# Kernel optimization log

Hardware: AMD Instinct MI355X
Metric: run time of the kernel (lower is better)

## Reference

```python
import jax, jax.numpy as jnp
import numpy as np

N, R, E = 20000, 4, 40000
C_IN, C_EDGE, HID, OUT = 256, 128, 512, 256
H = 8
D = HID // H
SCALE = 1.0 / float(np.sqrt(D))


def _hgt_layer(x, src, dst, Wkqv, bkqv, Wk, Wv, prel, Wout, bout, skip):
    # x: [n, c_in]; src/dst: [R, E] int; Wk/Wv: [R, H, D, D]; prel: [R, H]
    n = x.shape[0]
    kqv = x @ Wkqv + bkqv                      # [n, 3*HID], split order k|q|v (torch.tensor_split)
    k, q, v = jnp.split(kqv, 3, axis=1)
    k = k.reshape(n, H, D)
    q = q.reshape(n, H, D)
    v = v.reshape(n, H, D)
    # per-(relation, head) DxD transforms (HeteroLinear k_rel / v_rel, no bias)
    k_rel = jnp.einsum('nhd,rhde->rnhe', k, Wk)   # [R, n, H, D]
    v_rel = jnp.einsum('nhd,rhde->rnhe', v, Wv)
    gather = jax.vmap(lambda t, i: t[i])          # per-relation gather
    k_e = gather(k_rel, src)                      # [R, E, H, D]
    v_e = gather(v_rel, src)
    q_e = q[dst]                                  # [R, E, H, D]
    alpha = jnp.einsum('rehd,rehd->reh', q_e, k_e) * prel[:, None, :] * SCALE
    m = src.shape[0] * src.shape[1]
    alpha = alpha.reshape(m, H)
    dstf = dst.reshape(m)
    # segment softmax over destination nodes, jointly across all relations
    amax = jax.ops.segment_max(alpha, dstf, num_segments=n)      # [n, H]
    ae = jnp.exp(alpha - amax[dstf])
    denom = jax.ops.segment_sum(ae, dstf, num_segments=n)
    w = ae / (denom[dstf] + 1e-16)
    msg = (v_e.reshape(m, H, D) * w[:, :, None]).reshape(m, H * D)
    agg = jax.ops.segment_sum(msg, dstf, num_segments=n)          # [n, HID]
    out = jax.nn.gelu(agg, approximate=False) @ Wout + bout
    if skip is not None:  # sigmoid-gated residual, only when dims match
        a = jax.nn.sigmoid(skip)
        out = a * out + (1.0 - a) * x
    return out


def setup_inputs() -> dict:
    key = jax.random.key(0)
    ks = jax.random.split(key, 16)
    def g(k, shape, fan):
        return jax.random.normal(k, shape, jnp.float32) / np.sqrt(fan)
    inp = {
        'x': jax.random.normal(ks[0], (N, C_IN), jnp.float32),
        'edge_index': jax.random.randint(ks[1], (R, 2, E), 0, N),
        'edge_attr': jax.random.normal(ks[2], (R, E, C_EDGE), jnp.float32),
        'Wkqv0': g(ks[3], (C_IN, 3 * HID), C_IN), 'bkqv0': jnp.zeros((3 * HID,), jnp.float32),
        'Wk0': g(ks[4], (R, H, D, D), D), 'Wv0': g(ks[5], (R, H, D, D), D),
        'prel0': jnp.ones((R, H), jnp.float32),
        'Wout0': g(ks[6], (HID, HID), HID), 'bout0': jnp.zeros((HID,), jnp.float32),
        'Wkqv1': g(ks[7], (HID, 3 * HID), HID), 'bkqv1': jnp.zeros((3 * HID,), jnp.float32),
        'Wk1': g(ks[8], (R, H, D, D), D), 'Wv1': g(ks[9], (R, H, D, D), D),
        'prel1': jnp.ones((R, H), jnp.float32),
        'Wout1': g(ks[10], (HID, HID), HID), 'bout1': jnp.zeros((HID,), jnp.float32),
        'skip1': jnp.ones((), jnp.float32),
        'Wfc': g(ks[11], (HID, OUT), HID), 'bfc': jnp.zeros((OUT,), jnp.float32),
        'We1': g(ks[12], (C_EDGE, HID), C_EDGE), 'be1': jnp.zeros((HID,), jnp.float32),
        'We2': g(ks[13], (HID, OUT), HID), 'be2': jnp.zeros((OUT,), jnp.float32),
    }
    return inp


def reference(x, edge_index, edge_attr, Wkqv0, bkqv0, Wk0, Wv0, prel0, Wout0, bout0, Wkqv1, bkqv1, Wk1, Wv1, prel1, Wout1, bout1, skip1, Wfc, bfc, We1, be1, We2, be2):
    src = edge_index[:, 0, :]
    dst = edge_index[:, 1, :]
    h = _hgt_layer(x, src, dst, Wkqv0, bkqv0, Wk0, Wv0, prel0, Wout0, bout0, None)
    h = _hgt_layer(h, src, dst, Wkqv1, bkqv1, Wk1, Wv1, prel1, Wout1, bout1, skip1)
    node_embeds = h @ Wfc + bfc
    e = edge_attr.reshape(R * E, C_EDGE)  # concat over relations
    edge_embeds = jax.nn.relu(e @ We1 + be1) @ We2 + be2
    return node_embeds, edge_embeds
```

## Files before the change

### kernel.cpp

```cpp
#include <hip/hip_runtime.h>
#include <cstdint>
#include <cstddef>

#define NN      20000
#define RR      4
#define EE      40000
#define CIN     256
#define CEDGE   128
#define HIDW    512
#define OUTW    256
#define NH      8
#define MEDGE   (RR*EE)
#define SCALEF  0.125f

typedef unsigned short u16;
typedef short s8v  __attribute__((ext_vector_type(8)));
typedef float f32x4 __attribute__((ext_vector_type(4)));

#define B_KQV   10240000ull
#define B_KREL  71680000ull
#define B_AGG   153600000ull
#define B_H0    174080000ull
#define B_H1    194560000ull
#define B_ALPHA 215040000ull
#define B_LSE   220160000ull
#define B_ROWP  220800000ull
#define B_EREC  220880128ull
#define B_WTS   221520128ull
#define B_EINT  0ull
#define WS_NEED 227000000ull

#define SZH ((size_t)NN * 256)

__device__ __forceinline__ u16 f2b(float f) {
    unsigned u = __float_as_uint(f);
    unsigned r = (u + 0x7FFFu + ((u >> 16) & 1u)) >> 16;
    return (u16)r;
}
__device__ __forceinline__ float b2f(u16 h) { return __uint_as_float(((unsigned)h) << 16); }
__device__ __forceinline__ float gelu_exact(float x) {
    return 0.5f * x * (1.0f + erff(x * 0.70710678118654752f));
}

__device__ __forceinline__ void gl_lds16(const u16* g, u16* l) {
    __builtin_amdgcn_global_load_lds(
        (const __attribute__((address_space(1))) void*)g,
        (__attribute__((address_space(3))) void*)l, 16, 0, 0);
}

template<int BN, int ACT, bool OUTBF16, bool BIAS, bool SKIP, bool AF32 = false>
__global__ __launch_bounds__(256) void gemm_bf16(
    const void* __restrict__ Av, int lda, size_t astride,
    const u16* __restrict__ BT, int ldb, size_t bstride,
    const float* __restrict__ bias,
    void* __restrict__ Cv, int ldc, size_t cstride,
    int M, int K,
    const u16* __restrict__ skipx, const float* __restrict__ gatep)
{
    constexpr int FN = BN / 32;
    constexpr int BI = BN / 32;
    __shared__ __align__(16) u16 As[128 * 64];
    __shared__ __align__(16) u16 Bs[BN * 64];

    const int t = threadIdx.x, lane = t & 63, wid = t >> 6;
    const int m0 = blockIdx.y * 128, n0 = blockIdx.x * BN;
    const int z  = blockIdx.z;
    const u16*   Bz = BT + (size_t)z * bstride;
    const float* Af = (const float*)Av + (AF32 ? (size_t)z * astride : 0);
    const u16*   Au = (const u16*)Av   + (AF32 ? 0 : (size_t)z * astride);
    const int wm = wid >> 1, wn = wid & 1;

    const int srow   = lane >> 3;
    const int schunk = (lane & 7) ^ srow;

    f32x4 acc[4][FN];
    #pragma unroll
    for (int i = 0; i < 4; ++i)
        #pragma unroll
        for (int j = 0; j < FN; ++j)
            acc[i][j] = (f32x4){0.f, 0.f, 0.f, 0.f};

    for (int k0 = 0; k0 < K; k0 += 64) {
        if (AF32) {
            #pragma unroll
            for (int i = 0; i < 4; ++i) {
                int c = i * 256 + t;
                int row = c >> 3, cc = c & 7;
                int gr = m0 + row; gr = gr < M ? gr : M - 1;
                const float* Ap = Af + (size_t)gr * lda + k0 + cc * 8;
                float4 p = *(const float4*)Ap;
                float4 q = *(const float4*)(Ap + 4);
                s8v v;
                v[0] = (short)f2b(p.x); v[1] = (short)f2b(p.y);
                v[2] = (short)f2b(p.z); v[3] = (short)f2b(p.w);
                v[4] = (short)f2b(q.x); v[5] = (short)f2b(q.y);
                v[6] = (short)f2b(q.z); v[7] = (short)f2b(q.w);
                *(s8v*)&As[row * 64 + ((cc ^ (row & 7)) << 3)] = v;
            }
        } else {
            #pragma unroll
            for (int i = 0; i < 4; ++i) {
                int t4 = wid * 4 + i;
                int row = t4 * 8 + srow;
                int gr = m0 + row; gr = gr < M ? gr : M - 1;
                gl_lds16(Au + (size_t)gr * lda + k0 + schunk * 8, &As[t4 * 512]);
            }
        }
        #pragma unroll
        for (int i = 0; i < BI; ++i) {
            int tb = wid * BI + i;
            int col = n0 + tb * 8 + srow;
            gl_lds16(Bz + (size_t)col * ldb + k0 + schunk * 8, &Bs[tb * 512]);
        }
        __syncthreads();
        #pragma unroll
        for (int ks = 0; ks < 2; ++ks) {
            s8v af[4], bf[FN];
            #pragma unroll
            for (int i = 0; i < 4; ++i) {
                int arow = wm * 64 + i * 16 + (lane & 15);
                int ac   = (ks * 4 + (lane >> 4)) ^ (lane & 7);
                af[i] = *(const s8v*)&As[arow * 64 + ac * 8];
            }
            #pragma unroll
            for (int j = 0; j < FN; ++j) {
                int brow = wn * (BN / 2) + j * 16 + (lane & 15);
                int bc   = (ks * 4 + (lane >> 4)) ^ (lane & 7);
                bf[j] = *(const s8v*)&Bs[brow * 64 + bc * 8];
            }
            #pragma unroll
            for (int i = 0; i < 4; ++i)
                #pragma unroll
                for (int j = 0; j < FN; ++j)
                    acc[i][j] = __builtin_amdgcn_mfma_f32_16x16x32_bf16(af[i], bf[j], acc[i][j], 0, 0, 0);
        }
        __syncthreads();
    }

    float gate = 1.f, ogate = 0.f;
    if (SKIP) { float s = *gatep; gate = 1.f / (1.f + expf(-s)); ogate = 1.f - gate; }
    u16*   Cb = (u16*)Cv   + (size_t)z * cstride;
    float* Cf = (float*)Cv + (size_t)z * cstride;
    #pragma unroll
    for (int i = 0; i < 4; ++i) {
        int rbase = m0 + wm * 64 + i * 16 + (lane >> 4) * 4;
        #pragma unroll
        for (int j = 0; j < FN; ++j) {
            int col = n0 + wn * (BN / 2) + j * 16 + (lane & 15);
            float bv = BIAS ? bias[col] : 0.f;
            #pragma unroll
            for (int q = 0; q < 4; ++q) {
                int r = rbase + q;
                if (r >= M) continue;
                float v = acc[i][j][q] + bv;
                if (ACT == 1) v = fmaxf(v, 0.f);
                if (ACT == 2) v = gelu_exact(v);
                if (SKIP) v = gate * v + ogate * b2f(skipx[(size_t)r * ldc + col]);
                if (OUTBF16) Cb[(size_t)r * ldc + col] = f2b(v);
                else         Cf[(size_t)r * ldc + col] = v;
            }
        }
    }
}

__global__ __launch_bounds__(256) void transpose_f2b(
    const float* __restrict__ W, u16* __restrict__ WT, int K, int N)
{
    __shared__ float tile[32][33];
    int kb = blockIdx.x * 32, nb = blockIdx.y * 32;
    int tx = threadIdx.x & 31, ty = threadIdx.x >> 5;
    #pragma unroll
    for (int i = 0; i < 32; i += 8)
        tile[ty + i][tx] = W[(size_t)(kb + ty + i) * N + nb + tx];
    __syncthreads();
    #pragma unroll
    for (int i = 0; i < 32; i += 8)
        WT[(size_t)(nb + ty + i) * K + kb + tx] = f2b(tile[tx][ty + i]);
}

__global__ void conv_wk(const float* __restrict__ Wk, u16* __restrict__ WkT)
{
    int idx = blockIdx.x * 256 + threadIdx.x;
    if (idx >= 8 * 256 * 64) return;
    int d = idx & 63, re = (idx >> 6) & 255, h = idx >> 14;
    int e = re & 63, r = re >> 6;
    WkT[idx] = f2b(Wk[(size_t)(((r * 8 + h) * 64 + d) * 64) + e]);
}

__global__ void conv_wv(const float* __restrict__ Wv, u16* __restrict__ WvT)
{
    int idx = blockIdx.x * 256 + threadIdx.x;
    if (idx >= 8 * 64 * 256) return;
    int d = idx & 63, r = (idx >> 6) & 3, e = (idx >> 8) & 63, h = idx >> 14;
    WvT[idx] = f2b(Wv[(size_t)(((r * 8 + h) * 64 + d) * 64) + e]);
}

__global__ void deg_kernel(const int* __restrict__ ei, int* __restrict__ rowptr)
{
    int idx = blockIdx.x * 256 + threadIdx.x;
    if (idx >= MEDGE) return;
    int r = idx / EE;
    atomicAdd(&rowptr[ei[idx + (r + 1) * EE]], 1);
}

__global__ __launch_bounds__(256) void scan_kernel(int* __restrict__ rowptr)
{
    __shared__ int buf[256];
    __shared__ int carry;
    const int t = threadIdx.x;
    if (t == 0) carry = 0;
    __syncthreads();
    for (int base = 0; base < NN; base += 256) {
        int i = base + t;
        int v = (i < NN) ? rowptr[i] : 0;
        buf[t] = v;
        __syncthreads();
        for (int off = 1; off < 256; off <<= 1) {
            int tv = (t >= off) ? buf[t - off] : 0;
            __syncthreads();
            buf[t] += tv;
            __syncthreads();
        }
        int total = buf[255];
        int excl = buf[t] - v;
        int c = carry;
        __syncthreads();
        if (i < NN) rowptr[i] = c + excl;
        if (t == 0) carry = c + total;
        __syncthreads();
    }
    if (t == 0) rowptr[NN] = carry;
}

__global__ void fill_kernel(const int* __restrict__ ei, const int* __restrict__ rowptr,
                            int* __restrict__ fillcnt, int* __restrict__ erec)
{
    int idx = blockIdx.x * 256 + threadIdx.x;
    if (idx >= MEDGE) return;
    int r = idx / EE;
    int dst = ei[idx + (r + 1) * EE];
    int pos = rowptr[dst] + atomicAdd(&fillcnt[dst], 1);
    erec[pos] = idx;
}

__global__ __launch_bounds__(256) void alpha_stats(
    const u16* __restrict__ krel2, const u16* __restrict__ kqvb,
    const int* __restrict__ ei, const int* __restrict__ rowptr,
    const int* __restrict__ erec, const float* __restrict__ prel,
    float* __restrict__ alpha, float* __restrict__ lse)
{
    int n    = (blockIdx.x * 256 + threadIdx.x) >> 6;
    int lane = threadIdx.x & 63;
    if (n >= NN) return;
    int p0 = rowptr[n], p1 = rowptr[n + 1];
    int h = lane >> 3, sub = lane & 7;
    s8v qv = *(const s8v*)(kqvb + (size_t)n * 1536 + 512 + h * 64 + sub * 8);
    float qf[8];
    #pragma unroll
    for (int q = 0; q < 8; ++q) qf[q] = b2f((u16)qv[q]);
    float m = -3.0e38f, ssum = 0.f;
    for (int j = p0; j < p1; ++j) {
        int idx = erec[j];
        int r = idx / EE;
        int src = ei[idx + r * EE];
        s8v kv = *(const s8v*)(krel2 + (size_t)src * 2048 + h * 256 + r * 64 + sub * 8);
        float s = 0.f;
        #pragma unroll
        for (int q = 0; q < 8; ++q) s += b2f((u16)kv[q]) * qf[q];
        s += __shfl_xor(s, 1);
        s += __shfl_xor(s, 2);
        s += __shfl_xor(s, 4);
        float a = s * prel[r * NH + h] * SCALEF;
        if (sub == 0) alpha[(size_t)idx * 8 + h] = a;
        float mn = fmaxf(m, a);
        ssum = ssum * expf(m - mn) + expf(a - mn);
        m = mn;
    }
    if (sub == 0) lse[(size_t)n * 8 + h] = m + logf(ssum + 1e-16f);
}

__global__ __launch_bounds__(256) void wsum_all(
    const u16* __restrict__ kqvb, const float* __restrict__ alpha,
    const float* __restrict__ lse, const int* __restrict__ rowptr,
    const int* __restrict__ erec, const int* __restrict__ ei,
    u16* __restrict__ wsumH)
{
    int n    = (blockIdx.x * 256 + threadIdx.x) >> 6;
    int lane = threadIdx.x & 63;
    if (n >= NN) return;
    int p0 = rowptr[n], p1 = rowptr[n + 1];
    int h = lane >> 3;
    float ls = lse[(size_t)n * 8 + h];
    float a0[8] = {}, a1[8] = {}, a2[8] = {}, a3[8] = {};
    for (int j = p0; j < p1; ++j) {
        int idx = erec[j];
        int r = idx / EE;
        int src = ei[idx + r * EE];
        float w = expf(alpha[(size_t)idx * 8 + h] - ls);
        s8v vv = *(const s8v*)(kqvb + (size_t)src * 1536 + 1024 + lane * 8);
        if (r == 0) {
            #pragma unroll
            for (int q = 0; q < 8; ++q) a0[q] += w * b2f((u16)vv[q]);
        } else if (r == 1) {
            #pragma unroll
            for (int q = 0; q < 8; ++q) a1[q] += w * b2f((u16)vv[q]);
        } else if (r == 2) {
            #pragma unroll
            for (int q = 0; q < 8; ++q) a2[q] += w * b2f((u16)vv[q]);
        } else {
            #pragma unroll
            for (int q = 0; q < 8; ++q) a3[q] += w * b2f((u16)vv[q]);
        }
    }
    u16* base = wsumH + (size_t)h * SZH + (size_t)n * 256 + (lane & 7) * 8;
    s8v o;
    #pragma unroll
    for (int q = 0; q < 8; ++q) o[q] = (short)f2b(a0[q]);
    *(s8v*)(base + 0)   = o;
    #pragma unroll
    for (int q = 0; q < 8; ++q) o[q] = (short)f2b(a1[q]);
    *(s8v*)(base + 64)  = o;
    #pragma unroll
    for (int q = 0; q < 8; ++q) o[q] = (short)f2b(a2[q]);
    *(s8v*)(base + 128) = o;
    #pragma unroll
    for (int q = 0; q < 8; ++q) o[q] = (short)f2b(a3[q]);
    *(s8v*)(base + 192) = o;
}

extern "C" void kernel_launch(void* const* d_in, const int* in_sizes, int n_in,
                              void* d_out, int out_size, void* d_ws, size_t ws_size,
                              hipStream_t stream)
{
    const float* x    = (const float*)d_in[0];
    const int*   ei   = (const int*)d_in[1];
    const float* ea   = (const float*)d_in[2];
    const float* Wkqv[2] = {(const float*)d_in[3],  (const float*)d_in[10]};
    const float* bkqv[2] = {(const float*)d_in[4],  (const float*)d_in[11]};
    const float* Wk[2]   = {(const float*)d_in[5],  (const float*)d_in[12]};
    const float* Wv[2]   = {(const float*)d_in[6],  (const float*)d_in[13]};
    const float* prel[2] = {(const float*)d_in[7],  (const float*)d_in[14]};
    const float* Wout[2] = {(const float*)d_in[8],  (const float*)d_in[15]};
    const float* bout[2] = {(const float*)d_in[9],  (const float*)d_in[16]};
    const float* skip1 = (const float*)d_in[17];
    const float* Wfc   = (const float*)d_in[18];
    const float* bfc   = (const float*)d_in[19];
    const float* We1   = (const float*)d_in[20];
    const float* be1   = (const float*)d_in[21];
    const float* We2   = (const float*)d_in[22];
    const float* be2   = (const float*)d_in[23];

    if (ws_size < WS_NEED) return;

    char* wsb = (char*)d_ws;
    u16*   kqvb  = (u16*)(wsb + B_KQV);
    u16*   krel2 = (u16*)(wsb + B_KREL);
    u16*   wsumH = krel2;
    u16*   aggb  = (u16*)(wsb + B_AGG);
    u16*   h0b   = (u16*)(wsb + B_H0);
    u16*   h1b   = (u16*)(wsb + B_H1);
    float* alpha = (float*)(wsb + B_ALPHA);
    float* lse   = (float*)(wsb + B_LSE);
    int*   fillcnt = (int*)(wsb + B_LSE);
    int*   rowptr  = (int*)(wsb + B_ROWP);
    int*   erec    = (int*)(wsb + B_EREC);
    u16*   eintb = (u16*)(wsb + B_EINT);
    float* outf  = (float*)d_out;

    u16* wt = (u16*)(wsb + B_WTS);
    u16* WkqvT[2] = {wt, wt + 393216};              wt += 393216 + 786432;
    u16* WkT[2]   = {wt, wt + 131072};              wt += 262144;
    u16* WvT[2]   = {wt, wt + 131072};              wt += 262144;
    u16* WoutT[2] = {wt, wt + 262144};              wt += 524288;
    u16* WfcT     = wt;                             wt += 131072;
    u16* We1T     = wt;                             wt += 65536;
    u16* We2T     = wt;

    const dim3 blk(256);
    const int mt128  = (NN + 127) / 128;
    const int mtE    = MEDGE / 128;

    transpose_f2b<<<dim3(CIN / 32, 1536 / 32), blk, 0, stream>>>(Wkqv[0], WkqvT[0], CIN, 1536);
    transpose_f2b<<<dim3(HIDW / 32, 1536 / 32), blk, 0, stream>>>(Wkqv[1], WkqvT[1], HIDW, 1536);
    transpose_f2b<<<dim3(HIDW / 32, HIDW / 32), blk, 0, stream>>>(Wout[0], WoutT[0], HIDW, HIDW);
    transpose_f2b<<<dim3(HIDW / 32, HIDW / 32), blk, 0, stream>>>(Wout[1], WoutT[1], HIDW, HIDW);
    transpose_f2b<<<dim3(HIDW / 32, OUTW / 32), blk, 0, stream>>>(Wfc, WfcT, HIDW, OUTW);
    transpose_f2b<<<dim3(CEDGE / 32, HIDW / 32), blk, 0, stream>>>(We1, We1T, CEDGE, HIDW);
    transpose_f2b<<<dim3(HIDW / 32, OUTW / 32), blk, 0, stream>>>(We2, We2T, HIDW, OUTW);
    for (int l = 0; l < 2; ++l) {
        conv_wk<<<(131072 + 255) / 256, blk, 0, stream>>>(Wk[l], WkT[l]);
        conv_wv<<<(131072 + 255) / 256, blk, 0, stream>>>(Wv[l], WvT[l]);
    }

    hipMemsetAsync(rowptr, 0, (NN + 1) * sizeof(int), stream);
    hipMemsetAsync(fillcnt, 0, NN * sizeof(int), stream);
    deg_kernel<<<(MEDGE + 255) / 256, blk, 0, stream>>>(ei, rowptr);
    scan_kernel<<<1, blk, 0, stream>>>(rowptr);
    fill_kernel<<<(MEDGE + 255) / 256, blk, 0, stream>>>(ei, rowptr, fillcnt, erec);

    for (int l = 0; l < 2; ++l) {
        int K = (l == 0) ? CIN : HIDW;

        if (l == 0)
            gemm_bf16<128, 0, true, true, false, true><<<dim3(12, mt128), blk, 0, stream>>>(
                (const void*)x, K, 0, WkqvT[0], K, 0, bkqv[0], kqvb, 1536, 0, NN, K, nullptr, nullptr);
        else
            gemm_bf16<128, 0, true, true, false><<<dim3(12, mt128), blk, 0, stream>>>(
                (const void*)h0b, K, 0, WkqvT[1], K, 0, bkqv[1], kqvb, 1536, 0, NN, K, nullptr, nullptr);

        gemm_bf16<128, 0, true, false, false><<<dim3(2, mt128, NH), blk, 0, stream>>>(
            (const void*)kqvb, 1536, 64, WkT[l], 64, (size_t)256 * 64, nullptr,
            krel2, 2048, 256, NN, 64, nullptr, nullptr);

        alpha_stats<<<(NN * 64) / 256, blk, 0, stream>>>(
            krel2, kqvb, ei, rowptr, erec, prel[l], alpha, lse);

        wsum_all<<<(NN * 64) / 256, blk, 0, stream>>>(
            kqvb, alpha, lse, rowptr, erec, ei, wsumH);

        gemm_bf16<64, 2, true, false, false><<<dim3(1, mt128, NH), blk, 0, stream>>>(
            (const void*)wsumH, 256, SZH, WvT[l], 256, (size_t)64 * 256, nullptr,
            aggb, 512, 64, NN, 256, nullptr, nullptr);

        if (l == 0)
            gemm_bf16<128, 0, true, true, false><<<dim3(4, mt128), blk, 0, stream>>>(
                (const void*)aggb, 512, 0, WoutT[0], 512, 0, bout[0], h0b, 512, 0, NN, 512, nullptr, nullptr);
        else
            gemm_bf16<128, 0, true, true, true><<<dim3(4, mt128), blk, 0, stream>>>(
                (const void*)aggb, 512, 0, WoutT[1], 512, 0, bout[1], h1b, 512, 0, NN, 512, h0b, skip1);
    }

    gemm_bf16<128, 0, false, true, false><<<dim3(2, mt128), blk, 0, stream>>>(
        (const void*)h1b, 512, 0, WfcT, 512, 0, bfc, outf, 256, 0, NN, 512, nullptr, nullptr);

    gemm_bf16<128, 1, true, true, false, true><<<dim3(4, mtE), blk, 0, stream>>>(
        (const void*)ea, 128, 0, We1T, 128, 0, be1, eintb, 512, 0, MEDGE, 128, nullptr, nullptr);
    gemm_bf16<128, 0, false, true, false><<<dim3(2, mtE), blk, 0, stream>>>(
        (const void*)eintb, 512, 0, We2T, 512, 0, be2,
        outf + 5120000, 256, 0, MEDGE, 512, nullptr, nullptr);
}
```

Measured before the change: 844.1 us.

## Fuse two-layer edge MLP into one kernel keeping the hidden tile in LDS

The two edge GEMMs (relu(e@We1+be1) and the second projection @We2+be2) are replaced by one kernel. Each block processes 64 edges and produces the 512-wide hidden activation in 128-column chunks in LDS, so the second GEMM consumes it directly. This removes the write and re-read of the 160000x512 bf16 intermediate through global memory and one launch. The cost is that B fragments are read straight from global memory without LDS staging, and the small 64-row tile gives less weight reuse per block.

```diff
diff --git a/kernel.cpp b/kernel.cpp
--- a/kernel.cpp
+++ b/kernel.cpp
@@ -27,7 +27,6 @@
 #define B_ROWP  220800000ull
 #define B_EREC  220880128ull
 #define B_WTS   221520128ull
-#define B_EINT  0ull
 #define WS_NEED 227000000ull
 
 #define SZH ((size_t)NN * 256)
@@ -158,6 +157,121 @@
                 if (SKIP) v = gate * v + ogate * b2f(skipx[(size_t)r * ldc + col]);
                 if (OUTBF16) Cb[(size_t)r * ldc + col] = f2b(v);
                 else         Cf[(size_t)r * ldc + col] = v;
+            }
+        }
+    }
+}
+
+__global__ __launch_bounds__(256) void edge_mlp(
+    const float* __restrict__ ea, const u16* __restrict__ We1T,
+    const float* __restrict__ b1, const u16* __restrict__ We2T,
+    const float* __restrict__ b2, float* __restrict__ out)
+{
+    __shared__ __align__(16) u16 Ae[64 * 128];
+    __shared__ __align__(16) u16 Ic[64 * 128];
+
+    const int t = threadIdx.x, lane = t & 63, w = t >> 6;
+    const int e0 = blockIdx.x * 64;
+    const int l15 = lane & 15, l4 = lane >> 4;
+
+    #pragma unroll
+    for (int i = 0; i < 4; ++i) {
+        int c = i * 256 + t;
+        int row = c >> 4, cc = c & 15;
+        const float* Ap = ea + (size_t)(e0 + row) * 128 + cc * 8;
+        float4 p = *(const float4*)Ap;
+        float4 q = *(const float4*)(Ap + 4);
+        s8v v;
+        v[0] = (short)f2b(p.x); v[1] = (short)f2b(p.y);
+        v[2] = (short)f2b(p.z); v[3] = (short)f2b(p.w);
+        v[4] = (short)f2b(q.x); v[5] = (short)f2b(q.y);
+        v[6] = (short)f2b(q.z); v[7] = (short)f2b(q.w);
+        *(s8v*)&Ae[row * 128 + ((cc ^ (row & 7)) << 3)] = v;
+    }
+    __syncthreads();
+
+    f32x4 acc2[4][4];
+    #pragma unroll
+    for (int m = 0; m < 4; ++m)
+        #pragma unroll
+        for (int n = 0; n < 4; ++n)
+            acc2[m][n] = (f32x4){0.f, 0.f, 0.f, 0.f};
+
+    for (int c = 0; c < 4; ++c) {
+        f32x4 sacc[4][2];
+        #pragma unroll
+        for (int m = 0; m < 4; ++m)
+            #pragma unroll
+            for (int n = 0; n < 2; ++n)
+                sacc[m][n] = (f32x4){0.f, 0.f, 0.f, 0.f};
+        #pragma unroll
+        for (int ks = 0; ks < 4; ++ks) {
+            s8v af[4], bf[2];
+            #pragma unroll
+            for (int m = 0; m < 4; ++m) {
+                int row = m * 16 + l15;
+                int kc  = (ks * 4 + l4) ^ (row & 7);
+                af[m] = *(const s8v*)&Ae[row * 128 + kc * 8];
+            }
+            #pragma unroll
+            for (int n = 0; n < 2; ++n) {
+                int col1 = c * 128 + w * 32 + n * 16 + l15;
+                bf[n] = *(const s8v*)(We1T + (size_t)col1 * 128 + ks * 32 + l4 * 8);
+            }
+            #pragma unroll
+            for (int m = 0; m < 4; ++m)
+                #pragma unroll
+                for (int n = 0; n < 2; ++n)
+                    sacc[m][n] = __builtin_amdgcn_mfma_f32_16x16x32_bf16(af[m], bf[n], sacc[m][n], 0, 0, 0);
+        }
+        __syncthreads();
+        #pragma unroll
+        for (int m = 0; m < 4; ++m) {
+            #pragma unroll
+            for (int n = 0; n < 2; ++n) {
+                int col = w * 32 + n * 16 + l15;
+                float bv = b1[c * 128 + col];
+                #pragma unroll
+                for (int q = 0; q < 4; ++q) {
+                    int row = m * 16 + l4 * 4 + q;
+                    float v = fmaxf(sacc[m][n][q] + bv, 0.f);
+                    Ic[row * 128 + (((col >> 3) ^ (row & 7)) << 3) + (col & 7)] = f2b(v);
+                }
+            }
+        }
+        __syncthreads();
+        #pragma unroll
+        for (int ks = 0; ks < 4; ++ks) {
+            s8v af[4], bf[4];
+            #pragma unroll
+            for (int m = 0; m < 4; ++m) {
+                int row = m * 16 + l15;
+                int kc  = (ks * 4 + l4) ^ (row & 7);
+                af[m] = *(const s8v*)&Ic[row * 128 + kc * 8];
+            }
+            #pragma unroll
+            for (int n = 0; n < 4; ++n) {
+                int col = w * 64 + n * 16 + l15;
+                bf[n] = *(const s8v*)(We2T + (size_t)col * 512 + c * 128 + ks * 32 + l4 * 8);
+            }
+            #pragma unroll
+            for (int m = 0; m < 4; ++m)
+                #pragma unroll
+                for (int n = 0; n < 4; ++n)
+                    acc2[m][n] = __builtin_amdgcn_mfma_f32_16x16x32_bf16(af[m], bf[n], acc2[m][n], 0, 0, 0);
+        }
+    }
+
+    #pragma unroll
+    for (int m = 0; m < 4; ++m) {
+        #pragma unroll
+        for (int n = 0; n < 4; ++n) {
+            int col = w * 64 + n * 16 + l15;
+            float bv = b2[col];
+            #pragma unroll
+            for (int q = 0; q < 4; ++q) {
+                int row = m * 16 + l4 * 4 + q;
+                out[(size_t)(e0 + row) * 256 + col] = acc2[m][n][q] + bv;
             }
         }
     }
@@ -364,7 +478,6 @@
     int*   fillcnt = (int*)(wsb + B_LSE);
     int*   rowptr  = (int*)(wsb + B_ROWP);
     int*   erec    = (int*)(wsb + B_EREC);
-    u16*   eintb = (u16*)(wsb + B_EINT);
     float* outf  = (float*)d_out;
 
     u16* wt = (u16*)(wsb + B_WTS);
@@ -378,7 +491,6 @@
 
     const dim3 blk(256);
     const int mt128  = (NN + 127) / 128;
-    const int mtE    = MEDGE / 128;
 
     transpose_f2b<<<dim3(CIN / 32, 1536 / 32), blk, 0, stream>>>(Wkqv[0], WkqvT[0], CIN, 1536);
     transpose_f2b<<<dim3(HIDW / 32, 1536 / 32), blk, 0, stream>>>(Wkqv[1], WkqvT[1], HIDW, 1536);
@@ -433,9 +545,5 @@
     gemm_bf16<128, 0, false, true, false><<<dim3(2, mt128), blk, 0, stream>>>(
         (const void*)h1b, 512, 0, WfcT, 512, 0, bfc, outf, 256, 0, NN, 512, nullptr, nullptr);
 
-    gemm_bf16<128, 1, true, true, false, true><<<dim3(4, mtE), blk, 0, stream>>>(
-        (const void*)ea, 128, 0, We1T, 128, 0, be1, eintb, 512, 0, MEDGE, 128, nullptr, nullptr);
-    gemm_bf16<128, 0, false, true, false><<<dim3(2, mtE), blk, 0, stream>>>(
-        (const void*)eintb, 512, 0, We2T, 512, 0, be2,
-        outf + 5120000, 256, 0, MEDGE, 512, nullptr, nullptr);
-}
+    edge_mlp<<<MEDGE / 64, blk, 0, stream>>>(ea, We1T, be1, We2T, be2, outf + 5120000);
+}
```

After: 762.7 us. 1.11x faster.

## Fuse edge MLP into one kernel keeping hidden activations in LDS

Applied to the files above, without the earlier changes.

Replaces the two-GEMM edge MLP (relu(ea@We1+b1)@We2+b2) with a single kernel in which each wave processes 16 edge rows. The 512-wide hidden layer is computed in 128-column chunks, stored as bf16 in LDS, and immediately consumed by the second GEMM. This removes the 160000x512 bf16 intermediate write and read to global memory and one kernel launch. In exchange, weight fragments are read straight from global/L2 by every wave without LDS tiling, so weight traffic and latency rise and MFMA utilisation may fall compared with the tiled GEMM.

```diff
diff --git a/kernel.cpp b/kernel.cpp
--- a/kernel.cpp
+++ b/kernel.cpp
@@ -27,7 +27,6 @@
 #define B_ROWP  220800000ull
 #define B_EREC  220880128ull
 #define B_WTS   221520128ull
-#define B_EINT  0ull
 #define WS_NEED 227000000ull
 
 #define SZH ((size_t)NN * 256)
@@ -159,6 +158,91 @@
                 if (OUTBF16) Cb[(size_t)r * ldc + col] = f2b(v);
                 else         Cf[(size_t)r * ldc + col] = v;
             }
+        }
+    }
+}
+
+__global__ __launch_bounds__(256) void edge_mlp(
+    const float* __restrict__ ea, const u16* __restrict__ We1T,
+    const float* __restrict__ b1, const u16* __restrict__ We2T,
+    const float* __restrict__ b2, float* __restrict__ out)
+{
+    __shared__ __align__(16) u16 AeAll[4][16 * 128];
+    __shared__ __align__(16) u16 IcAll[4][16 * 128];
+
+    const int t = threadIdx.x, lane = t & 63, w = t >> 6;
+    u16* Ae = AeAll[w];
+    u16* Ic = IcAll[w];
+    const int r0 = blockIdx.x * 64 + w * 16;
+    const int l15 = lane & 15, l4 = lane >> 4;
+
+    #pragma unroll
+    for (int i = 0; i < 8; ++i) {
+        int f   = i * 64 + lane;
+        int row = f >> 5;
+        int c4  = f & 31;
+        float4 p = *(const float4*)(ea + (size_t)(r0 + row) * 128 + c4 * 4);
+        unsigned lo = (unsigned)f2b(p.x) | ((unsigned)f2b(p.y) << 16);
+        unsigned hi = (unsigned)f2b(p.z) | ((unsigned)f2b(p.w) << 16);
+        int chunk = c4 >> 1;
+        int sub   = (c4 & 1) * 8;
+        *(uint2*)((char*)Ae + row * 256 + ((chunk ^ (row & 7)) << 4) + sub)
+            = make_uint2(lo, hi);
+    }
+
+    f32x4 acc2[16];
+    #pragma unroll
+    for (int n = 0; n < 16; ++n) acc2[n] = (f32x4){0.f, 0.f, 0.f, 0.f};
+
+    #pragma unroll
+    for (int c = 0; c < 4; ++c) {
+        f32x4 sacc[8];
+        #pragma unroll
+        for (int n = 0; n < 8; ++n) sacc[n] = (f32x4){0.f, 0.f, 0.f, 0.f};
+        #pragma unroll
+        for (int ks = 0; ks < 4; ++ks) {
+            int kc = (ks * 4 + l4) ^ (l15 & 7);
+            s8v af = *(const s8v*)&Ae[l15 * 128 + kc * 8];
+            #pragma unroll
+            for (int n = 0; n < 8; ++n) {
+                int col1 = c * 128 + n * 16 + l15;
+                s8v bf = *(const s8v*)(We1T + (size_t)col1 * 128 + ks * 32 + l4 * 8);
+                sacc[n] = __builtin_amdgcn_mfma_f32_16x16x32_bf16(af, bf, sacc[n], 0, 0, 0);
+            }
+        }
+        #pragma unroll
+        for (int n = 0; n < 8; ++n) {
+            int col = n * 16 + l15;
+            float bv = b1[c * 128 + col];
+            int chunk = col >> 3, sub = col & 7;
+            #pragma unroll
+            for (int q = 0; q < 4; ++q) {
+                int row = l4 * 4 + q;
+                float v = fmaxf(sacc[n][q] + bv, 0.f);
+                Ic[row * 128 + ((chunk ^ (row & 7)) << 3) + sub] = f2b(v);
+            }
+        }
+        #pragma unroll
+        for (int ks = 0; ks < 4; ++ks) {
+            int kc = (ks * 4 + l4) ^ (l15 & 7);
+            s8v af = *(const s8v*)&Ic[l15 * 128 + kc * 8];
+            #pragma unroll
+            for (int n = 0; n < 16; ++n) {
+                int col = n * 16 + l15;
+                s8v bf = *(const s8v*)(We2T + (size_t)col * 512 + c * 128 + ks * 32 + l4 * 8);
+                acc2[n] = __builtin_amdgcn_mfma_f32_16x16x32_bf16(af, bf, acc2[n], 0, 0, 0);
+            }
+        }
+    }
+
+    #pragma unroll
+    for (int n = 0; n < 16; ++n) {
+        int col = n * 16 + l15;
+        float bv = b2[col];
+        #pragma unroll
+        for (int q = 0; q < 4; ++q) {
+            int row = l4 * 4 + q;
+            out[(size_t)(r0 + row) * 256 + col] = acc2[n][q] + bv;
         }
     }
 }
@@ -364,7 +448,6 @@
     int*   fillcnt = (int*)(wsb + B_LSE);
     int*   rowptr  = (int*)(wsb + B_ROWP);
     int*   erec    = (int*)(wsb + B_EREC);
-    u16*   eintb = (u16*)(wsb + B_EINT);
     float* outf  = (float*)d_out;
 
     u16* wt = (u16*)(wsb + B_WTS);
@@ -378,7 +461,6 @@
 
     const dim3 blk(256);
     const int mt128  = (NN + 127) / 128;
-    const int mtE    = MEDGE / 128;
 
     transpose_f2b<<<dim3(CIN / 32, 1536 / 32), blk, 0, stream>>>(Wkqv[0], WkqvT[0], CIN, 1536);
     transpose_f2b<<<dim3(HIDW / 32, 1536 / 32), blk, 0, stream>>>(Wkqv[1], WkqvT[1], HIDW, 1536);
@@ -433,9 +515,5 @@
     gemm_bf16<128, 0, false, true, false><<<dim3(2, mt128), blk, 0, stream>>>(
         (const void*)h1b, 512, 0, WfcT, 512, 0, bfc, outf, 256, 0, NN, 512, nullptr, nullptr);
 
-    gemm_bf16<128, 1, true, true, false, true><<<dim3(4, mtE), blk, 0, stream>>>(
-        (const void*)ea, 128, 0, We1T, 128, 0, be1, eintb, 512, 0, MEDGE, 128, nullptr, nullptr);
-    gemm_bf16<128, 0, false, true, false><<<dim3(2, mtE), blk, 0, stream>>>(
-        (const void*)eintb, 512, 0, We2T, 512, 0, be2,
-        outf + 5120000, 256, 0, MEDGE, 512, nullptr, nullptr);
-}
+    edge_mlp<<<MEDGE / 64, blk, 0, stream>>>(ea, We1T, be1, We2T, be2, outf + 5120000);
+}
```

Measured after the change: 1.078 ms. 27.7% more time.
